# Kernel optimization log

Measured on AMD Instinct MI355X. Metric: run time of the kernel, lower is better.

## Reference

```python
import jax, jax.numpy as jnp
import numpy as np

D_MODEL = 1024

def setup_inputs() -> dict:
    key = jax.random.key(0)
    ks = jax.random.split(key, 7)
    s = 1.0 / np.sqrt(D_MODEL)
    x = jax.random.normal(ks[0], (4, 2048, D_MODEL), dtype=jnp.float32)
    wq_w = jax.random.uniform(ks[1], (D_MODEL, D_MODEL), jnp.float32, -s, s)
    wq_b = jax.random.uniform(ks[2], (D_MODEL,), jnp.float32, -s, s)
    wk_w = jax.random.uniform(ks[3], (D_MODEL, D_MODEL), jnp.float32, -s, s)
    wk_b = jax.random.uniform(ks[4], (D_MODEL,), jnp.float32, -s, s)
    wv_w = jax.random.uniform(ks[5], (D_MODEL, D_MODEL), jnp.float32, -s, s)
    wv_b = jax.random.uniform(ks[6], (D_MODEL,), jnp.float32, -s, s)
    return {"x": x, "wq_w": wq_w, "wq_b": wq_b, "wk_w": wk_w, "wk_b": wk_b, "wv_w": wv_w, "wv_b": wv_b}

def reference(x, wq_w, wq_b, wk_w, wk_b, wv_w, wv_b):
    # Linear: x @ W^T + b (torch nn.Linear convention)
    q = jnp.einsum('bsd,ed->bse', x, wq_w) + wq_b
    k = jnp.einsum('bsd,ed->bse', x, wk_w) + wk_b
    v = jnp.einsum('bsd,ed->bse', x, wv_w) + wv_b
    scale = 1.0 / jnp.sqrt(jnp.asarray(k.shape[-1], dtype=q.dtype))
    logits = jnp.einsum('bqd,bkd->bqk', q, k) * scale  # [B, S, S]
    attn = jax.nn.softmax(logits, axis=-1)
    out = jnp.einsum('bqk,bkd->bqd', attn, v)
    return (attn, out)
```

## Files before the change

### kernel.cpp

```cpp
#include <hip/hip_runtime.h>

typedef unsigned short u16;
typedef u16 u16x4 __attribute__((ext_vector_type(4)));
typedef u16 u16x8 __attribute__((ext_vector_type(8)));
typedef __bf16 bf16x8 __attribute__((ext_vector_type(8)));
typedef float f32x4 __attribute__((ext_vector_type(4)));
typedef float f32x16 __attribute__((ext_vector_type(16)));

static __device__ __forceinline__ u16 f2bf(float f) {
  unsigned u = __builtin_bit_cast(unsigned, f);
  u += 0x7fffu + ((u >> 16) & 1u);
  return (u16)(u >> 16);
}
static __device__ __forceinline__ float bf2f(u16 h) {
  return __builtin_bit_cast(float, ((unsigned)h) << 16);
}

static __device__ __forceinline__ void gload_lds16(const u16* g, u16* l) {
  u16* gn = const_cast<u16*>(g);
  __builtin_amdgcn_global_load_lds(
      (__attribute__((address_space(1))) unsigned int*)gn,
      (__attribute__((address_space(3))) unsigned int*)l,
      16, 0, 0);
}

__global__ __launch_bounds__(256)
void cvt_f32_bf16(const float* __restrict__ in, u16* __restrict__ out) {
  const int i = blockIdx.x * 256 + threadIdx.x;
  float4 f = ((const float4*)in)[i];
  u16x4 o = { f2bf(f.x), f2bf(f.y), f2bf(f.z), f2bf(f.w) };
  ((u16x4*)out)[i] = o;
}

__global__ __launch_bounds__(256)
void cvt_w3(const float* __restrict__ a, const float* __restrict__ b,
            const float* __restrict__ c, u16* __restrict__ out) {
  const int blk = blockIdx.x;
  const int w = blk >> 10;
  const float* src = (w == 0) ? a : (w == 1) ? b : c;
  const int i = (blk & 1023) * 256 + threadIdx.x;
  float4 f = ((const float4*)src)[i];
  u16x4 o = { f2bf(f.x), f2bf(f.y), f2bf(f.z), f2bf(f.w) };
  ((u16x4*)(out + (size_t)w * 1048576ULL))[i] = o;
}


#define MM16(a, b, c) __builtin_amdgcn_mfma_f32_16x16x32_bf16(a, b, c, 0, 0, 0)

#define STAGE_A(BUF, KH, KT) do {                                            \
    gload_lds16(Asrc + (KT) + (KH) * 32,                                     \
                AsW + (BUF) * 16384 + (KH) * 8192);                          \
    gload_lds16(Asrc + (size_t)128 * lda + (KT) + (KH) * 32,                 \
                AsW + (BUF) * 16384 + (KH) * 8192 + 4096);                   \
  } while (0)
#define STAGE_B(BUF, KH, KT) do {                                            \
    gload_lds16(Bsrc + (KT) + (KH) * 32,                                     \
                BsW + (BUF) * 16384 + (KH) * 8192);                          \
    gload_lds16(Bsrc + (size_t)128 * ldb + (KT) + (KH) * 32,                 \
                BsW + (BUF) * 16384 + (KH) * 8192 + 4096);                   \
  } while (0)

#define APTR(BUF, MI, KS) \
  ((const bf16x8*)(ArdBase + (BUF) * 16384 + (KS) * 8192 + (MI) * 512))
#define BPTR(BUF, NI, KS) \
  ((const bf16x8*)(BrdBase + (BUF) * 16384 + (KS) * 8192 + (NI) * 512))

#define VM4   asm volatile("s_waitcnt vmcnt(4)" ::: "memory")
#define NOVM  (void)0

#define PH(BUF, MH, KS, RDB, STG, VMW) do {                                  \
    bf16x8 a0 = *APTR(BUF, (MH) * 4 + 0, KS);                                \
    bf16x8 a1 = *APTR(BUF, (MH) * 4 + 1, KS);                                \
    bf16x8 a2 = *APTR(BUF, (MH) * 4 + 2, KS);                                \
    bf16x8 a3 = *APTR(BUF, (MH) * 4 + 3, KS);                                \
    if (RDB) {                                                               \
      bf0 = *BPTR(BUF, 0, KS);                                               \
      bf1 = *BPTR(BUF, 1, KS);                                               \
      bf2 = *BPTR(BUF, 2, KS);                                               \
      bf3 = *BPTR(BUF, 3, KS);                                               \
    }                                                                        \
    STG;                                                                     \
    __builtin_amdgcn_s_barrier();                                            \
    asm volatile("s_waitcnt lgkmcnt(0)" ::: "memory");                       \
    __builtin_amdgcn_sched_barrier(0);                                       \
    __builtin_amdgcn_s_setprio(1);                                           \
    acc[(MH)*4+0][0] = MM16(a0, bf0, acc[(MH)*4+0][0]);                      \
    acc[(MH)*4+1][0] = MM16(a1, bf0, acc[(MH)*4+1][0]);                      \
    acc[(MH)*4+2][0] = MM16(a2, bf0, acc[(MH)*4+2][0]);                      \
    acc[(MH)*4+3][0] = MM16(a3, bf0, acc[(MH)*4+3][0]);                      \
    acc[(MH)*4+0][1] = MM16(a0, bf1, acc[(MH)*4+0][1]);                      \
    acc[(MH)*4+1][1] = MM16(a1, bf1, acc[(MH)*4+1][1]);                      \
    acc[(MH)*4+2][1] = MM16(a2, bf1, acc[(MH)*4+2][1]);                      \
    acc[(MH)*4+3][1] = MM16(a3, bf1, acc[(MH)*4+3][1]);                      \
    acc[(MH)*4+0][2] = MM16(a0, bf2, acc[(MH)*4+0][2]);                      \
    acc[(MH)*4+1][2] = MM16(a1, bf2, acc[(MH)*4+1][2]);                      \
    acc[(MH)*4+2][2] = MM16(a2, bf2, acc[(MH)*4+2][2]);                      \
    acc[(MH)*4+3][2] = MM16(a3, bf2, acc[(MH)*4+3][2]);                      \
    acc[(MH)*4+0][3] = MM16(a0, bf3, acc[(MH)*4+0][3]);                      \
    acc[(MH)*4+1][3] = MM16(a1, bf3, acc[(MH)*4+1][3]);                      \
    acc[(MH)*4+2][3] = MM16(a2, bf3, acc[(MH)*4+2][3]);                      \
    acc[(MH)*4+3][3] = MM16(a3, bf3, acc[(MH)*4+3][3]);                      \
    __builtin_amdgcn_s_setprio(0);                                           \
    VMW;                                                                     \
    __builtin_amdgcn_sched_barrier(0);                                       \
    __builtin_amdgcn_s_barrier();                                            \
  } while (0)

template<int MODE>
__global__ __launch_bounds__(512, 1)
void gemm8p(const u16* __restrict__ Ain, const u16* __restrict__ Bin,
            void* __restrict__ Cv,
            const float* __restrict__ b0, const float* __restrict__ b1,
            const float* __restrict__ b2,
            int lda, int ldb, int ldc, int K,
            unsigned long long sA, unsigned long long sB, unsigned long long sC,
            int nbx, int nby)
{
  __shared__ alignas(16) u16 As[2 * 2 * 256 * 32];
  __shared__ alignas(16) u16 Bs[2 * 2 * 256 * 32];

  const int nbxy = nbx * nby;
  const int bid  = blockIdx.x;
  const int flat = (bid & 7) * ((int)gridDim.x >> 3) + (bid >> 3);
  const int z    = flat / nbxy;
  const int rr   = flat - z * nbxy;
  const int width = nbx << 3;
  const int gid  = rr / width;
  const int rw   = rr - gid * width;
  const int by   = (gid << 3) + (rw & 7);
  const int bx   = rw >> 3;

  const u16* A = Ain + z * sA;
  const u16* B = Bin + z * sB;

  const int tid  = threadIdx.x;
  const int wave = tid >> 6;
  const int lane = tid & 63;
  const int wr   = wave >> 2;
  const int wc   = wave & 3;
  const int l16  = lane & 15;
  const int l4   = lane >> 4;

  const int m0 = by << 8;
  const int n0 = bx << 8;

  const int gch = (tid & 3) ^ ((tid >> 3) & 3);
  const u16* Asrc = A + (size_t)(m0 + (tid >> 2)) * lda + gch * 8;
  const u16* Bsrc = B + (size_t)(n0 + (tid >> 2)) * ldb + gch * 8;
  u16* AsW = As + tid * 8;
  u16* BsW = Bs + tid * 8;

  const int rsw = (l4 ^ ((l16 >> 1) & 3)) << 3;
  const u16* ArdBase = As + (size_t)(wr * 128 + l16) * 32 + rsw;
  const u16* BrdBase = Bs + (size_t)(wc * 64 + l16) * 32 + rsw;

  f32x4 acc[8][4];
  #pragma unroll
  for (int i = 0; i < 8; ++i)
    #pragma unroll
    for (int j = 0; j < 4; ++j)
      #pragma unroll
      for (int r = 0; r < 4; ++r)
        acc[i][j][r] = 0.f;

  bf16x8 bf0, bf1, bf2, bf3;

  STAGE_A(0, 0, 0);  STAGE_B(0, 0, 0);
  STAGE_A(0, 1, 0);  STAGE_B(0, 1, 0);
  STAGE_A(1, 0, 64); STAGE_B(1, 0, 64);
  VM4;
  __builtin_amdgcn_sched_barrier(0);
  __builtin_amdgcn_s_barrier();

  const int NT = K >> 6;
  for (int t = 0; t < NT; t += 2) {
    const int kt1 = (t + 1) * 64;
    const int kt2 = (t + 2 < NT) ? (t + 2) * 64 : 0;
    const int kt3 = (t + 3 < NT) ? (t + 3) * 64 : 0;
    PH(0, 0, 0, 1, STAGE_A(1, 1, kt1), NOVM);
    PH(0, 1, 0, 0, STAGE_B(1, 1, kt1), NOVM);
    PH(0, 0, 1, 1, STAGE_A(0, 0, kt2), NOVM);
    PH(0, 1, 1, 0, STAGE_B(0, 0, kt2), VM4);
    PH(1, 0, 0, 1, STAGE_A(0, 1, kt2), NOVM);
    PH(1, 1, 0, 0, STAGE_B(0, 1, kt2), NOVM);
    PH(1, 0, 1, 1, STAGE_A(1, 0, kt3), NOVM);
    PH(1, 1, 1, 0, STAGE_B(1, 0, kt3), VM4);
  }
  asm volatile("s_waitcnt vmcnt(0)" ::: "memory");

  if constexpr (MODE == 0) {
    const int g = n0 >> 10;
    const int colb = (n0 + wc * 64) & 1023;
    const int rowb = m0 + wr * 128 + l4 * 4;
    if (g < 2) {
      u16* Cb = (u16*)Cv + (size_t)g * 8388608ULL;
      const float* bp = (g == 0) ? b0 : b1;
      const float qs = (g == 0) ? 0.03125f : 1.0f;
      #pragma unroll
      for (int ni = 0; ni < 4; ++ni) {
        const int col = colb + ni * 16 + l16;
        const float bv = bp[col];
        #pragma unroll
        for (int mi = 0; mi < 8; ++mi) {
          const int row = rowb + mi * 16;
          #pragma unroll
          for (int r = 0; r < 4; ++r)
            Cb[(size_t)(row + r) * 1024 + col] = f2bf((acc[mi][ni][r] + bv) * qs);
        }
      }
    } else {
      u16* Vt = (u16*)Cv + 16777216ULL;
      #pragma unroll
      for (int ni = 0; ni < 4; ++ni) {
        const int col = colb + ni * 16 + l16;
        const float bv = b2[col];
        #pragma unroll
        for (int mi = 0; mi < 8; ++mi) {
          const int row = rowb + mi * 16;
          u16x4 o;
          #pragma unroll
          for (int r = 0; r < 4; ++r) o[r] = f2bf(acc[mi][ni][r] + bv);
          const size_t idx = ((size_t)((row >> 11) * 1024 + col)) * 2048 + (row & 2047);
          *(u16x4*)&Vt[idx] = o;
        }
      }
    }
  } else {
    u16* Cb = (u16*)Cv + (size_t)z * sC;
    #pragma unroll
    for (int ni = 0; ni < 4; ++ni) {
      const int col = n0 + wc * 64 + ni * 16 + l16;
      #pragma unroll
      for (int mi = 0; mi < 8; ++mi) {
        const int row = m0 + wr * 128 + mi * 16 + l4 * 4;
        #pragma unroll
        for (int r = 0; r < 4; ++r)
          Cb[(size_t)(row + r) * ldc + col] = f2bf(acc[mi][ni][r]);
      }
    }
  }
}

template<int MODE>
__global__ __launch_bounds__(256)
void gemm_bt(const u16* __restrict__ Ain, const u16* __restrict__ Bin,
             void* __restrict__ Cv,
             int lda, int ldb, int ldc, int K,
             unsigned long long sA, unsigned long long sB, unsigned long long sC,
             int nbx, int nby)
{
  constexpr int BM = 128, BK = 64;
  __shared__ alignas(16) u16 As[BM * BK];
  __shared__ alignas(16) u16 Bs[BM * BK];

  const int nbxy = nbx * nby;
  const int bid  = blockIdx.x;
  const int flat = (bid & 7) * ((int)gridDim.x >> 3) + (bid >> 3);
  const int z    = flat / nbxy;
  const int rr   = flat - z * nbxy;
  const int width = nbx << 3;
  const int gid  = rr / width;
  const int rw   = rr - gid * width;
  const int by   = (gid << 3) + (rw & 7);
  const int bx   = rw >> 3;

  const u16* A = Ain + z * sA;
  const u16* B = Bin + z * sB;

  const int tid  = threadIdx.x;
  const int wave = tid >> 6;
  const int lane = tid & 63;
  const int l32  = lane & 31;
  const int half = lane >> 5;
  const int wr   = wave >> 1;
  const int wc   = wave & 1;

  const int m0 = by * BM;
  const int n0 = bx * BM;

  const int lr = lane >> 3;
  const int sc = ((lane & 7) ^ lr) * 8;
  const u16* Ag = A + (size_t)(m0 + wave * 32 + lr) * lda + sc;
  const u16* Bg = B + (size_t)(n0 + wave * 32 + lr) * ldb + sc;
  u16* Asb = &As[(wave * 32) * BK];
  u16* Bsb = &Bs[(wave * 32) * BK];

  f32x16 acc[2][2];
  #pragma unroll
  for (int i = 0; i < 2; ++i)
    #pragma unroll
    for (int j = 0; j < 2; ++j)
      #pragma unroll
      for (int r = 0; r < 16; ++r)
        acc[i][j][r] = 0.f;

  for (int k0 = 0; k0 < K; k0 += BK) {
    gload_lds16(Ag + k0,                    Asb);
    gload_lds16(Ag + (size_t) 8 * lda + k0, Asb +  8 * BK);
    gload_lds16(Ag + (size_t)16 * lda + k0, Asb + 16 * BK);
    gload_lds16(Ag + (size_t)24 * lda + k0, Asb + 24 * BK);
    gload_lds16(Bg + k0,                    Bsb);
    gload_lds16(Bg + (size_t) 8 * ldb + k0, Bsb +  8 * BK);
    gload_lds16(Bg + (size_t)16 * ldb + k0, Bsb + 16 * BK);
    gload_lds16(Bg + (size_t)24 * ldb + k0, Bsb + 24 * BK);
    __syncthreads();

    #pragma unroll
    for (int ks = 0; ks < 4; ++ks) {
      bf16x8 af[2], bfr[2];
      #pragma unroll
      for (int ti = 0; ti < 2; ++ti) {
        const int row = wr * 64 + ti * 32 + l32;
        const int ch  = ((ks * 2 + half) ^ (row & 7)) * 8;
        af[ti] = *(const bf16x8*)&As[row * BK + ch];
      }
      #pragma unroll
      for (int tj = 0; tj < 2; ++tj) {
        const int row = wc * 64 + tj * 32 + l32;
        const int ch  = ((ks * 2 + half) ^ (row & 7)) * 8;
        bfr[tj] = *(const bf16x8*)&Bs[row * BK + ch];
      }
      #pragma unroll
      for (int ti = 0; ti < 2; ++ti)
        #pragma unroll
        for (int tj = 0; tj < 2; ++tj)
          acc[ti][tj] = __builtin_amdgcn_mfma_f32_32x32x16_bf16(af[ti], bfr[tj], acc[ti][tj], 0, 0, 0);
    }
    __syncthreads();
  }

  const int colb = n0 + wc * 64 + l32;
  const int rowb = m0 + wr * 64 + 4 * half;

  if constexpr (MODE == 3) {
    float* Cf = (float*)Cv + z * sC;
    #pragma unroll
    for (int tj = 0; tj < 2; ++tj) {
      const int col = colb + tj * 32;
      #pragma unroll
      for (int ti = 0; ti < 2; ++ti)
        #pragma unroll
        for (int g4 = 0; g4 < 4; ++g4)
          #pragma unroll
          for (int r = 0; r < 4; ++r) {
            const int row = rowb + ti * 32 + g4 * 8 + r;
            Cf[(size_t)row * ldc + col] = acc[ti][tj][g4 * 4 + r];
          }
    }
  }
}

__global__ __launch_bounds__(256)
void softmax_rows(u16* __restrict__ logits, float* __restrict__ attn) {
  const int row = blockIdx.x;
  const int tid = threadIdx.x;
  u16*   lp = logits + (size_t)row * 2048 + tid * 8;
  float* ap = attn   + (size_t)row * 2048 + tid * 8;

  u16x8 raw = *(const u16x8*)lp;
  float v[8];
  #pragma unroll
  for (int j = 0; j < 8; ++j) v[j] = bf2f(raw[j]);

  float mx = v[0];
  #pragma unroll
  for (int j = 1; j < 8; ++j) mx = fmaxf(mx, v[j]);
  #pragma unroll
  for (int o = 32; o > 0; o >>= 1) mx = fmaxf(mx, __shfl_xor(mx, o, 64));

  __shared__ float smax[4], ssum[4];
  const int wv = tid >> 6, ln = tid & 63;
  if (ln == 0) smax[wv] = mx;
  __syncthreads();
  mx = fmaxf(fmaxf(smax[0], smax[1]), fmaxf(smax[2], smax[3]));

  float s = 0.f;
  #pragma unroll
  for (int j = 0; j < 8; ++j) { v[j] = __expf(v[j] - mx); s += v[j]; }
  #pragma unroll
  for (int o = 32; o > 0; o >>= 1) s += __shfl_xor(s, o, 64);
  if (ln == 0) ssum[wv] = s;
  __syncthreads();
  s = (ssum[0] + ssum[1]) + (ssum[2] + ssum[3]);
  const float inv = 1.f / s;

  u16x8 ob;
  #pragma unroll
  for (int j = 0; j < 8; ++j) { v[j] *= inv; ob[j] = f2bf(v[j]); }
  float4* apv = (float4*)ap;
  apv[0] = make_float4(v[0], v[1], v[2], v[3]);
  apv[1] = make_float4(v[4], v[5], v[6], v[7]);
  *(u16x8*)lp = ob;
}

extern "C" void kernel_launch(void* const* d_in, const int* in_sizes, int n_in,
                              void* d_out, int out_size, void* d_ws, size_t ws_size,
                              hipStream_t stream) {
  (void)in_sizes; (void)n_in; (void)out_size; (void)ws_size;
  const float* x    = (const float*)d_in[0];
  const float* wq_w = (const float*)d_in[1];
  const float* wq_b = (const float*)d_in[2];
  const float* wk_w = (const float*)d_in[3];
  const float* wk_b = (const float*)d_in[4];
  const float* wv_w = (const float*)d_in[5];
  const float* wv_b = (const float*)d_in[6];

  float* attn = (float*)d_out;
  float* outp = attn + 16777216ULL;

  u16* xb   = (u16*)d_ws;
  u16* wcat = xb   + 8388608ULL;
  u16* Qb   = wcat + 3145728ULL;
  u16* Kb   = Qb   + 8388608ULL;
  u16* Vt   = Kb   + 8388608ULL;
  u16* Lg   = Vt   + 8388608ULL;

  cvt_f32_bf16<<<8192, 256, 0, stream>>>(x, xb);
  cvt_w3<<<3072, 256, 0, stream>>>(wq_w, wk_w, wv_w, wcat);

  gemm8p<0><<<384, 512, 0, stream>>>(xb, wcat, Qb, wq_b, wk_b, wv_b,
                                     1024, 1024, 1024, 1024, 0, 0, 0, 12, 32);

  gemm8p<2><<<256, 512, 0, stream>>>(Qb, Kb, Lg, nullptr, nullptr, nullptr,
                                     1024, 1024, 2048, 1024,
                                     2097152ULL, 2097152ULL, 4194304ULL, 8, 8);

  softmax_rows<<<8192, 256, 0, stream>>>(Lg, attn);

  gemm_bt<3><<<512, 256, 0, stream>>>(Lg, Vt, outp,
                                      2048, 2048, 1024, 2048,
                                      4194304ULL, 2097152ULL, 2097152ULL, 8, 16);
}
```

Measured before the change: 314.2 us.

## Run QKV projection on smaller-tile GEMM and merge conversion kernels

The fused QKV projection moves from the large 256x256 pipelined kernel to the simpler 128x128 gemm_bt kernel, which now carries the bias/scale and V-transpose epilogue. This yields 1536 blocks instead of 384, avoiding the poor wave quantization of 1.5 blocks per CU at the cost of less data reuse and no software pipelining. The two f32-to-bf16 conversion kernels are merged into one launch to cut launch overhead.

New measurement: 312.1 us. About the same (-0.7%).

```diff
diff --git a/kernel.cpp b/kernel.cpp
--- a/kernel.cpp
+++ b/kernel.cpp
@@ -25,23 +25,175 @@
 }
 
 __global__ __launch_bounds__(256)
-void cvt_f32_bf16(const float* __restrict__ in, u16* __restrict__ out) {
-  const int i = blockIdx.x * 256 + threadIdx.x;
-  float4 f = ((const float4*)in)[i];
-  u16x4 o = { f2bf(f.x), f2bf(f.y), f2bf(f.z), f2bf(f.w) };
-  ((u16x4*)out)[i] = o;
-}
-
+void cvt_all(const float* __restrict__ x, u16* __restrict__ xb,
+             const float* __restrict__ a, const float* __restrict__ b,
+             const float* __restrict__ c, u16* __restrict__ wcat) {
+  const int blkid = blockIdx.x;
+  if (blkid < 8192) {
+    const int i = blkid * 256 + threadIdx.x;
+    float4 f = ((const float4*)x)[i];
+    u16x4 o = { f2bf(f.x), f2bf(f.y), f2bf(f.z), f2bf(f.w) };
+    ((u16x4*)xb)[i] = o;
+  } else {
+    const int blk = blkid - 8192;
+    const int w = blk >> 10;
+    const float* src = (w == 0) ? a : (w == 1) ? b : c;
+    const int i = (blk & 1023) * 256 + threadIdx.x;
+    float4 f = ((const float4*)src)[i];
+    u16x4 o = { f2bf(f.x), f2bf(f.y), f2bf(f.z), f2bf(f.w) };
+    ((u16x4*)(wcat + (size_t)w * 1048576ULL))[i] = o;
+  }
+}
+
+template<int MODE>
 __global__ __launch_bounds__(256)
-void cvt_w3(const float* __restrict__ a, const float* __restrict__ b,
-            const float* __restrict__ c, u16* __restrict__ out) {
-  const int blk = blockIdx.x;
-  const int w = blk >> 10;
-  const float* src = (w == 0) ? a : (w == 1) ? b : c;
-  const int i = (blk & 1023) * 256 + threadIdx.x;
-  float4 f = ((const float4*)src)[i];
-  u16x4 o = { f2bf(f.x), f2bf(f.y), f2bf(f.z), f2bf(f.w) };
-  ((u16x4*)(out + (size_t)w * 1048576ULL))[i] = o;
+void gemm_bt(const u16* __restrict__ Ain, const u16* __restrict__ Bin,
+             void* __restrict__ Cv,
+             const float* __restrict__ b0, const float* __restrict__ b1,
+             const float* __restrict__ b2,
+             int lda, int ldb, int ldc, int K,
+             unsigned long long sA, unsigned long long sB, unsigned long long sC,
+             int nbx, int nby)
+{
+  constexpr int BM = 128, BN = 128, BK = 64;
+  __shared__ alignas(16) u16 As[BM * BK];
+  __shared__ alignas(16) u16 Bs[BN * BK];
+
+  const int nbxy = nbx * nby;
+  const int bid  = blockIdx.x;
+  const int flat = (bid & 7) * ((int)gridDim.x >> 3) + (bid >> 3);
+  const int z    = flat / nbxy;
+  const int rr   = flat - z * nbxy;
+  const int width = nbx << 3;
+  const int gid  = rr / width;
+  const int rw   = rr - gid * width;
+  const int by   = (gid << 3) + (rw & 7);
+  const int bx   = rw >> 3;
+
+  const u16* A = Ain + z * sA;
+  const u16* B = Bin + z * sB;
+
+  const int tid  = threadIdx.x;
+  const int wave = tid >> 6;
+  const int lane = tid & 63;
+  const int l32  = lane & 31;
+  const int half = lane >> 5;
+  const int wr   = wave >> 1;
+  const int wc   = wave & 1;
+
+  const int m0 = by * BM;
+  const int n0 = bx * BN;
+
+  const int lr = lane >> 3;
+  const int sc = ((lane & 7) ^ lr) * 8;
+  const u16* Ag = A + (size_t)(m0 + wave * 32 + lr) * lda + sc;
+  const u16* Bg = B + (size_t)(n0 + wave * 32 + lr) * ldb + sc;
+  u16* Asb = &As[(wave * 32) * BK];
+  u16* Bsb = &Bs[(wave * 32) * BK];
+
+  f32x16 acc[2][2];
+  #pragma unroll
+  for (int i = 0; i < 2; ++i)
+    #pragma unroll
+    for (int j = 0; j < 2; ++j)
+      #pragma unroll
+      for (int r = 0; r < 16; ++r)
+        acc[i][j][r] = 0.f;
+
+  for (int k0 = 0; k0 < K; k0 += BK) {
+    gload_lds16(Ag + k0,                    Asb);
+    gload_lds16(Ag + (size_t) 8 * lda + k0, Asb +  8 * BK);
+    gload_lds16(Ag + (size_t)16 * lda + k0, Asb + 16 * BK);
+    gload_lds16(Ag + (size_t)24 * lda + k0, Asb + 24 * BK);
+    gload_lds16(Bg + k0,                    Bsb);
+    gload_lds16(Bg + (size_t) 8 * ldb + k0, Bsb +  8 * BK);
+    gload_lds16(Bg + (size_t)16 * ldb + k0, Bsb + 16 * BK);
+    gload_lds16(Bg + (size_t)24 * ldb + k0, Bsb + 24 * BK);
+    __syncthreads();
+
+    #pragma unroll
+    for (int ks = 0; ks < 4; ++ks) {
+      bf16x8 af[2], bfr[2];
+      #pragma unroll
+      for (int ti = 0; ti < 2; ++ti) {
+        const int row = wr * 64 + ti * 32 + l32;
+        const int ch  = ((ks * 2 + half) ^ (row & 7)) * 8;
+        af[ti] = *(const bf16x8*)&As[row * BK + ch];
+      }
+      #pragma unroll
+      for (int tj = 0; tj < 2; ++tj) {
+        const int row = wc * 64 + tj * 32 + l32;
+        const int ch  = ((ks * 2 + half) ^ (row & 7)) * 8;
+        bfr[tj] = *(const bf16x8*)&Bs[row * BK + ch];
+      }
+      #pragma unroll
+      for (int ti = 0; ti < 2; ++ti)
+        #pragma unroll
+        for (int tj = 0; tj < 2; ++tj)
+          acc[ti][tj] = __builtin_amdgcn_mfma_f32_32x32x16_bf16(af[ti], bfr[tj], acc[ti][tj], 0, 0, 0);
+    }
+    __syncthreads();
+  }
+
+  const int colb = n0 + wc * 64 + l32;
+  const int rowb = m0 + wr * 64 + 4 * half;
+
+  if constexpr (MODE == 0) {
+    const int g = n0 >> 10;
+    u16* Qb = (u16*)Cv;
+    if (g < 2) {
+      u16* Cb = Qb + (size_t)g * 8388608ULL;
+      const float* bp = (g == 0) ? b0 : b1;
+      const float qs = (g == 0) ? 0.03125f : 1.0f;
+      #pragma unroll
+      for (int tj = 0; tj < 2; ++tj) {
+        const int col = (colb + tj * 32) & 1023;
+        const float bv = bp[col];
+        #pragma unroll
+        for (int ti = 0; ti < 2; ++ti)
+          #pragma unroll
+          for (int g4 = 0; g4 < 4; ++g4)
+            #pragma unroll
+            for (int r = 0; r < 4; ++r) {
+              const int row = rowb + ti * 32 + g4 * 8 + r;
+              Cb[(size_t)row * 1024 + col] = f2bf((acc[ti][tj][g4 * 4 + r] + bv) * qs);
+            }
+      }
+    } else {
+      u16* Vt = Qb + 16777216ULL;
+      #pragma unroll
+      for (int tj = 0; tj < 2; ++tj) {
+        const int col = (colb + tj * 32) & 1023;
+        const float bv = b2[col];
+        #pragma unroll
+        for (int ti = 0; ti < 2; ++ti)
+          #pragma unroll
+          for (int g4 = 0; g4 < 4; ++g4) {
+            const int row = rowb + ti * 32 + g4 * 8;
+            u16x4 o;
+            #pragma unroll
+            for (int r = 0; r < 4; ++r) o[r] = f2bf(acc[ti][tj][g4 * 4 + r] + bv);
+            const size_t idx = ((size_t)((row >> 11) * 1024 + col)) * 2048 + (row & 2047);
+            *(u16x4*)&Vt[idx] = o;
+          }
+      }
+    }
+  } else {
+    float* Cf = (float*)Cv + z * sC;
+    #pragma unroll
+    for (int tj = 0; tj < 2; ++tj) {
+      const int col = colb + tj * 32;
+      #pragma unroll
+      for (int ti = 0; ti < 2; ++ti)
+        #pragma unroll
+        for (int g4 = 0; g4 < 4; ++g4)
+          #pragma unroll
+          for (int r = 0; r < 4; ++r) {
+            const int row = rowb + ti * 32 + g4 * 8 + r;
+            Cf[(size_t)row * ldc + col] = acc[ti][tj][g4 * 4 + r];
+          }
+    }
+  }
 }
 
 
@@ -110,8 +262,6 @@
 __global__ __launch_bounds__(512, 1)
 void gemm8p(const u16* __restrict__ Ain, const u16* __restrict__ Bin,
             void* __restrict__ Cv,
-            const float* __restrict__ b0, const float* __restrict__ b1,
-            const float* __restrict__ b2,
             int lda, int ldb, int ldc, int K,
             unsigned long long sA, unsigned long long sB, unsigned long long sC,
             int nbx, int nby)
@@ -188,164 +338,16 @@
   }
   asm volatile("s_waitcnt vmcnt(0)" ::: "memory");
 
-  if constexpr (MODE == 0) {
-    const int g = n0 >> 10;
-    const int colb = (n0 + wc * 64) & 1023;
-    const int rowb = m0 + wr * 128 + l4 * 4;
-    if (g < 2) {
-      u16* Cb = (u16*)Cv + (size_t)g * 8388608ULL;
-      const float* bp = (g == 0) ? b0 : b1;
-      const float qs = (g == 0) ? 0.03125f : 1.0f;
-      #pragma unroll
-      for (int ni = 0; ni < 4; ++ni) {
-        const int col = colb + ni * 16 + l16;
-        const float bv = bp[col];
-        #pragma unroll
-        for (int mi = 0; mi < 8; ++mi) {
-          const int row = rowb + mi * 16;
-          #pragma unroll
-          for (int r = 0; r < 4; ++r)
-            Cb[(size_t)(row + r) * 1024 + col] = f2bf((acc[mi][ni][r] + bv) * qs);
-        }
-      }
-    } else {
-      u16* Vt = (u16*)Cv + 16777216ULL;
-      #pragma unroll
-      for (int ni = 0; ni < 4; ++ni) {
-        const int col = colb + ni * 16 + l16;
-        const float bv = b2[col];
-        #pragma unroll
-        for (int mi = 0; mi < 8; ++mi) {
-          const int row = rowb + mi * 16;
-          u16x4 o;
-          #pragma unroll
-          for (int r = 0; r < 4; ++r) o[r] = f2bf(acc[mi][ni][r] + bv);
-          const size_t idx = ((size_t)((row >> 11) * 1024 + col)) * 2048 + (row & 2047);
-          *(u16x4*)&Vt[idx] = o;
-        }
-      }
-    }
-  } else {
-    u16* Cb = (u16*)Cv + (size_t)z * sC;
+  u16* Cb = (u16*)Cv + (size_t)z * sC;
+  #pragma unroll
+  for (int ni = 0; ni < 4; ++ni) {
+    const int col = n0 + wc * 64 + ni * 16 + l16;
     #pragma unroll
-    for (int ni = 0; ni < 4; ++ni) {
-      const int col = n0 + wc * 64 + ni * 16 + l16;
-      #pragma unroll
-      for (int mi = 0; mi < 8; ++mi) {
-        const int row = m0 + wr * 128 + mi * 16 + l4 * 4;
-        #pragma unroll
-        for (int r = 0; r < 4; ++r)
-          Cb[(size_t)(row + r) * ldc + col] = f2bf(acc[mi][ni][r]);
-      }
-    }
-  }
-}
-
-template<int MODE>
-__global__ __launch_bounds__(256)
-void gemm_bt(const u16* __restrict__ Ain, const u16* __restrict__ Bin,
-             void* __restrict__ Cv,
-             int lda, int ldb, int ldc, int K,
-             unsigned long long sA, unsigned long long sB, unsigned long long sC,
-             int nbx, int nby)
-{
-  constexpr int BM = 128, BK = 64;
-  __shared__ alignas(16) u16 As[BM * BK];
-  __shared__ alignas(16) u16 Bs[BM * BK];
-
-  const int nbxy = nbx * nby;
-  const int bid  = blockIdx.x;
-  const int flat = (bid & 7) * ((int)gridDim.x >> 3) + (bid >> 3);
-  const int z    = flat / nbxy;
-  const int rr   = flat - z * nbxy;
-  const int width = nbx << 3;
-  const int gid  = rr / width;
-  const int rw   = rr - gid * width;
-  const int by   = (gid << 3) + (rw & 7);
-  const int bx   = rw >> 3;
-
-  const u16* A = Ain + z * sA;
-  const u16* B = Bin + z * sB;
-
-  const int tid  = threadIdx.x;
-  const int wave = tid >> 6;
-  const int lane = tid & 63;
-  const int l32  = lane & 31;
-  const int half = lane >> 5;
-  const int wr   = wave >> 1;
-  const int wc   = wave & 1;
-
-  const int m0 = by * BM;
-  const int n0 = bx * BM;
-
-  const int lr = lane >> 3;
-  const int sc = ((lane & 7) ^ lr) * 8;
-  const u16* Ag = A + (size_t)(m0 + wave * 32 + lr) * lda + sc;
-  const u16* Bg = B + (size_t)(n0 + wave * 32 + lr) * ldb + sc;
-  u16* Asb = &As[(wave * 32) * BK];
-  u16* Bsb = &Bs[(wave * 32) * BK];
-
-  f32x16 acc[2][2];
-  #pragma unroll
-  for (int i = 0; i < 2; ++i)
-    #pragma unroll
-    for (int j = 0; j < 2; ++j)
-      #pragma unroll
-      for (int r = 0; r < 16; ++r)
-        acc[i][j][r] = 0.f;
-
-  for (int k0 = 0; k0 < K; k0 += BK) {
-    gload_lds16(Ag + k0,                    Asb);
-    gload_lds16(Ag + (size_t) 8 * lda + k0, Asb +  8 * BK);
-    gload_lds16(Ag + (size_t)16 * lda + k0, Asb + 16 * BK);
-    gload_lds16(Ag + (size_t)24 * lda + k0, Asb + 24 * BK);
-    gload_lds16(Bg + k0,                    Bsb);
-    gload_lds16(Bg + (size_t) 8 * ldb + k0, Bsb +  8 * BK);
-    gload_lds16(Bg + (size_t)16 * ldb + k0, Bsb + 16 * BK);
-    gload_lds16(Bg + (size_t)24 * ldb + k0, Bsb + 24 * BK);
-    __syncthreads();
-
-    #pragma unroll
-    for (int ks = 0; ks < 4; ++ks) {
-      bf16x8 af[2], bfr[2];
-      #pragma unroll
-      for (int ti = 0; ti < 2; ++ti) {
-        const int row = wr * 64 + ti * 32 + l32;
-        const int ch  = ((ks * 2 + half) ^ (row & 7)) * 8;
-        af[ti] = *(const bf16x8*)&As[row * BK + ch];
-      }
-      #pragma unroll
-      for (int tj = 0; tj < 2; ++tj) {
-        const int row = wc * 64 + tj * 32 + l32;
-        const int ch  = ((ks * 2 + half) ^ (row & 7)) * 8;
-        bfr[tj] = *(const bf16x8*)&Bs[row * BK + ch];
-      }
-      #pragma unroll
-      for (int ti = 0; ti < 2; ++ti)
-        #pragma unroll
-        for (int tj = 0; tj < 2; ++tj)
-          acc[ti][tj] = __builtin_amdgcn_mfma_f32_32x32x16_bf16(af[ti], bfr[tj], acc[ti][tj], 0, 0, 0);
-    }
-    __syncthreads();
-  }
-
-  const int colb = n0 + wc * 64 + l32;
-  const int rowb = m0 + wr * 64 + 4 * half;
-
-  if constexpr (MODE == 3) {
-    float* Cf = (float*)Cv + z * sC;
-    #pragma unroll
-    for (int tj = 0; tj < 2; ++tj) {
-      const int col = colb + tj * 32;
-      #pragma unroll
-      for (int ti = 0; ti < 2; ++ti)
-        #pragma unroll
-        for (int g4 = 0; g4 < 4; ++g4)
-          #pragma unroll
-          for (int r = 0; r < 4; ++r) {
-            const int row = rowb + ti * 32 + g4 * 8 + r;
-            Cf[(size_t)row * ldc + col] = acc[ti][tj][g4 * 4 + r];
-          }
+    for (int mi = 0; mi < 8; ++mi) {
+      const int row = m0 + wr * 128 + mi * 16 + l4 * 4;
+      #pragma unroll
+      for (int r = 0; r < 4; ++r)
+        Cb[(size_t)(row + r) * ldc + col] = f2bf(acc[mi][ni][r]);
     }
   }
 }
@@ -415,19 +417,18 @@
   u16* Vt   = Kb   + 8388608ULL;
   u16* Lg   = Vt   + 8388608ULL;
 
-  cvt_f32_bf16<<<8192, 256, 0, stream>>>(x, xb);
-  cvt_w3<<<3072, 256, 0, stream>>>(wq_w, wk_w, wv_w, wcat);
-
-  gemm8p<0><<<384, 512, 0, stream>>>(xb, wcat, Qb, wq_b, wk_b, wv_b,
-                                     1024, 1024, 1024, 1024, 0, 0, 0, 12, 32);
-
-  gemm8p<2><<<256, 512, 0, stream>>>(Qb, Kb, Lg, nullptr, nullptr, nullptr,
+  cvt_all<<<11264, 256, 0, stream>>>(x, xb, wq_w, wk_w, wv_w, wcat);
+
+  gemm_bt<0><<<1536, 256, 0, stream>>>(xb, wcat, Qb, wq_b, wk_b, wv_b,
+                                       1024, 1024, 1024, 1024, 0, 0, 0, 24, 64);
+
+  gemm8p<2><<<256, 512, 0, stream>>>(Qb, Kb, Lg,
                                      1024, 1024, 2048, 1024,
                                      2097152ULL, 2097152ULL, 4194304ULL, 8, 8);
 
   softmax_rows<<<8192, 256, 0, stream>>>(Lg, attn);
 
-  gemm_bt<3><<<512, 256, 0, stream>>>(Lg, Vt, outp,
+  gemm_bt<3><<<512, 256, 0, stream>>>(Lg, Vt, outp, nullptr, nullptr, nullptr,
                                       2048, 2048, 1024, 2048,
                                       4194304ULL, 2097152ULL, 2097152ULL, 8, 16);
 }
```
